# Kernel tuning notes

Hardware: AMD Instinct MI355X
Metric: run time of the kernel (lower is better)

Reference implementation:

```python
import jax, jax.numpy as jnp
import numpy as np

N_NODES = 50000
N_EDGES = 400000
N_GRAPHS = 64
DN = 64    # node features
DE = 64    # edge features
DG = 16    # global features
DH = 128   # mlp hidden
DO = 64    # mlp output
NHID = 2   # hidden layers
E_IN = 2 * DN + DE + DG   # 208
N_IN = DN + DO + DG       # 144


def _mlp_params(key, d_in, d_h, d_out, n_hid):
    ks = jax.random.split(key, 3)
    w_in = jax.random.normal(ks[0], (d_in, d_h), jnp.float32) * (2.0 / d_in) ** 0.5
    w_h = jax.random.normal(ks[1], (n_hid, d_h, d_h), jnp.float32) * (2.0 / d_h) ** 0.5
    w_out = jax.random.normal(ks[2], (d_h, d_out), jnp.float32) * (2.0 / d_h) ** 0.5
    return (w_in, jnp.zeros((d_h,), jnp.float32), w_h, jnp.zeros((n_hid, d_h), jnp.float32),
            w_out, jnp.zeros((d_out,), jnp.float32), jnp.ones((d_out,), jnp.float32),
            jnp.zeros((d_out,), jnp.float32))


def _mlp(h, w_in, b_in, w_h, b_h, w_out, b_out, g, b):
    # Lin -> [relu, Lin]*NHID -> relu -> Lin -> LayerNorm  (dropout=0 at eval)
    h = h @ w_in + b_in
    for i in range(w_h.shape[0]):
        h = jax.nn.relu(h) @ w_h[i] + b_h[i]
    h = jax.nn.relu(h) @ w_out + b_out
    mu = jnp.mean(h, axis=-1, keepdims=True)
    var = jnp.mean((h - mu) ** 2, axis=-1, keepdims=True)
    return (h - mu) * jax.lax.rsqrt(var + 1e-5) * g + b


def setup_inputs() -> dict:
    key = jax.random.key(0)
    k = jax.random.split(key, 8)
    x = jax.random.normal(k[0], (N_NODES, DN), jnp.float32)
    edge_attr = jax.random.normal(k[1], (N_EDGES, DE), jnp.float32)
    u = jax.random.normal(k[2], (N_GRAPHS, DG), jnp.float32)
    edge_index = jax.random.randint(k[3], (2, N_EDGES), 0, N_NODES, dtype=jnp.int32)
    batch = jnp.sort(jax.random.randint(k[4], (N_NODES,), 0, N_GRAPHS, dtype=jnp.int32))
    names = ["w_in", "b_in", "w_h", "b_h", "w_out", "b_out", "ln_g", "ln_b"]
    d = {"x": x, "edge_attr": edge_attr, "u": u, "edge_index": edge_index, "batch": batch}
    for pref, kk, d_in in (("e_", k[5], E_IN), ("a_", k[6], E_IN), ("n_", k[7], N_IN)):
        for nm, v in zip(names, _mlp_params(kk, d_in, DH, DO, NHID)):
            d[pref + nm] = v
    return d


def reference(x, edge_attr, u, edge_index, batch,
              e_w_in, e_b_in, e_w_h, e_b_h, e_w_out, e_b_out, e_ln_g, e_ln_b,
              a_w_in, a_b_in, a_w_h, a_b_h, a_w_out, a_b_out, a_ln_g, a_ln_b,
              n_w_in, n_b_in, n_w_h, n_b_h, n_w_out, n_b_out, n_ln_g, n_ln_b):
    src, tgt = edge_index[0], edge_index[1]
    edge_batch = batch[src]
    # EdgeModel: gather src/tgt node feats + global feats, concat, MLP (+ sigmoid attention MLP)
    neigh = jnp.concatenate([x[src], x[tgt], edge_attr, u[edge_batch]], axis=1)  # [E, E_IN]
    e_out = _mlp(neigh, e_w_in, e_b_in, e_w_h, e_b_h, e_w_out, e_b_out, e_ln_g, e_ln_b)
    attn = jax.nn.sigmoid(_mlp(neigh, a_w_in, a_b_in, a_w_h, a_b_h, a_w_out, a_b_out, a_ln_g, a_ln_b))
    e_out = e_out * attn  # [E, DO]
    # NodeModel: scatter-sum incoming (target-indexed) edge outputs, concat, MLP
    agg = jax.ops.segment_sum(e_out, tgt, num_segments=x.shape[0])  # [N, DO], zeros for isolated nodes
    node_in = jnp.concatenate([x, agg, u[batch]], axis=1)  # [N, N_IN]
    x_out = _mlp(node_in, n_w_in, n_b_in, n_w_h, n_b_h, n_w_out, n_b_out, n_ln_g, n_ln_b)
    return x_out
```

## Files before the change

kernel.cpp:

```cpp
#include <hip/hip_runtime.h>
#include <math.h>

#define N_NODES 50000
#define N_EDGES 400000

typedef _Float16 half8 __attribute__((ext_vector_type(8)));
typedef float f32x4 __attribute__((ext_vector_type(4)));

#define LD1 232
#define LDH 136
#define LDN 168

#define AGG_OFF 0
#define XH_OFF  12800000
#define UH_OFF  19200000
#define WP_OFF  19202048
#define O_EW1 0
#define O_EH0 28672
#define O_EH1 45056
#define O_EWO 61440
#define O_AW1 69632
#define O_AH0 98304
#define O_AH1 114688
#define O_AWO 131072
#define O_NW1 139264
#define O_NH0 159744
#define O_NH1 176128
#define O_NWO 192512

__device__ __forceinline__ f32x4 mfma16(half8 a, half8 b, f32x4 c) {
  return __builtin_amdgcn_mfma_f32_16x16x32_f16(a, b, c, 0, 0, 0);
}

template<int NS, int LDSRC>
__device__ __forceinline__ void gemm32(const _Float16* __restrict__ src,
                                       _Float16* __restrict__ dst,
                                       const _Float16* __restrict__ wp16,
                                       const float* __restrict__ bias,
                                       int w, int lane) {
  const half8* wp = (const half8*)wp16;
  const int r = lane & 15, ch = lane >> 4;
  f32x4 a0[4], a1[4];
#pragma unroll
  for (int m = 0; m < 4; ++m) {
    a0[m] = (f32x4){0.f, 0.f, 0.f, 0.f};
    a1[m] = (f32x4){0.f, 0.f, 0.f, 0.f};
  }
#pragma unroll
  for (int s = 0; s < NS; ++s) {
    half8 b0 = wp[(s * 4 + ch) * 128 + w * 32 + r];
    half8 b1 = wp[(s * 4 + ch) * 128 + w * 32 + 16 + r];
#pragma unroll
    for (int m = 0; m < 4; ++m) {
      half8 a = *(const half8*)(src + (m * 16 + r) * LDSRC + s * 32 + ch * 8);
      a0[m] = mfma16(a, b0, a0[m]);
      a1[m] = mfma16(a, b1, a1[m]);
    }
  }
  float bb0 = bias[w * 32 + r], bb1 = bias[w * 32 + 16 + r];
#pragma unroll
  for (int m = 0; m < 4; ++m)
#pragma unroll
    for (int q = 0; q < 4; ++q) {
      int row = m * 16 + ch * 4 + q;
      dst[row * LDH + w * 32 + r]      = (_Float16)fmaxf(a0[m][q] + bb0, 0.f);
      dst[row * LDH + w * 32 + 16 + r] = (_Float16)fmaxf(a1[m][q] + bb1, 0.f);
    }
}

struct EdgeP {
  const float* edge_attr; const int* edge_index; const int* batch;
  const _Float16* x_h; const _Float16* u_h; const _Float16* wp;
  const float *eBin, *eBh, *eBout, *eG, *eBt;
  const float *aBin, *aBh, *aBout, *aG, *aBt;
  float* agg;
};

__global__ __launch_bounds__(512, 4) void edge_kernel(EdgeP p) {
  __shared__ __align__(16) _Float16 sIn[64 * LD1];
  __shared__ __align__(16) _Float16 sQe[64 * LDH];
  __shared__ __align__(16) _Float16 sQa[64 * LDH];
  __shared__ __align__(16) _Float16 sPa[64 * LDH];
  const int tid = threadIdx.x;
  const int e0 = blockIdx.x * 64;

  for (int idx = tid; idx < 64 * 32; idx += 512) {
    int c = idx & 31, e = idx >> 5;
    if (c >= 28) continue;
    int col = c * 8;
    half8 v;
    if (col < 64) {
      int s = p.edge_index[e0 + e];
      v = *(const half8*)(p.x_h + (size_t)s * 64 + col);
    } else if (col < 128) {
      int t = p.edge_index[N_EDGES + e0 + e];
      v = *(const half8*)(p.x_h + (size_t)t * 64 + col - 64);
    } else if (col < 192) {
      const float* ea = p.edge_attr + (size_t)(e0 + e) * 64 + (col - 128);
      float4 f0 = *(const float4*)ea, f1 = *(const float4*)(ea + 4);
      v[0] = (_Float16)f0.x; v[1] = (_Float16)f0.y;
      v[2] = (_Float16)f0.z; v[3] = (_Float16)f0.w;
      v[4] = (_Float16)f1.x; v[5] = (_Float16)f1.y;
      v[6] = (_Float16)f1.z; v[7] = (_Float16)f1.w;
    } else if (col < 208) {
      int s = p.edge_index[e0 + e];
      int eb = p.batch[s];
      v = *(const half8*)(p.u_h + eb * 16 + col - 192);
    } else {
#pragma unroll
      for (int j = 0; j < 8; ++j) v[j] = (_Float16)0.f;
    }
    *(half8*)(sIn + e * LD1 + col) = v;
  }
  __syncthreads();

  const int lane = tid & 63, wid = tid >> 6, we = wid & 3;
  const bool isE = wid < 4;
  _Float16* ping = isE ? sQe : sQa;
  _Float16* pong = isE ? sIn : sPa;
  const _Float16* w1 = p.wp + (isE ? O_EW1 : O_AW1);
  const _Float16* h0 = p.wp + (isE ? O_EH0 : O_AH0);
  const _Float16* h1 = p.wp + (isE ? O_EH1 : O_AH1);
  const _Float16* wo = p.wp + (isE ? O_EWO : O_AWO);
  const float* bin = isE ? p.eBin : p.aBin;
  const float* bh  = isE ? p.eBh  : p.aBh;
  const float* bo  = isE ? p.eBout: p.aBout;
  const float* g   = isE ? p.eG   : p.aG;
  const float* bt  = isE ? p.eBt  : p.aBt;

  gemm32<7, LD1>(sIn,  ping, w1, bin,      we, lane); __syncthreads();
  gemm32<4, LDH>(ping, pong, h0, bh,       we, lane); __syncthreads();
  gemm32<4, LDH>(pong, ping, h1, bh + 128, we, lane); __syncthreads();

  const int r = lane & 15, ch = lane >> 4;
  const half8* wpo = (const half8*)wo;
  f32x4 acc[4];
#pragma unroll
  for (int t = 0; t < 4; ++t) acc[t] = (f32x4){0.f, 0.f, 0.f, 0.f};
#pragma unroll
  for (int s = 0; s < 4; ++s) {
    half8 a = *(const half8*)(ping + (we * 16 + r) * LDH + s * 32 + ch * 8);
#pragma unroll
    for (int t = 0; t < 4; ++t)
      acc[t] = mfma16(a, wpo[(s * 4 + ch) * 64 + t * 16 + r], acc[t]);
  }
  float gg[4], tt[4];
#pragma unroll
  for (int t = 0; t < 4; ++t) {
    int cidx = t * 16 + r;
    float bov = bo[cidx];
#pragma unroll
    for (int q = 0; q < 4; ++q) acc[t][q] += bov;
    gg[t] = g[cidx]; tt[t] = bt[cidx];
  }
  float mu_[4], rs_[4];
#pragma unroll
  for (int q = 0; q < 4; ++q) {
    float s1 = 0.f, s2 = 0.f;
#pragma unroll
    for (int t = 0; t < 4; ++t) { float v = acc[t][q]; s1 += v; s2 += v * v; }
#pragma unroll
    for (int mk = 1; mk < 16; mk <<= 1) {
      s1 += __shfl_xor(s1, mk); s2 += __shfl_xor(s2, mk);
    }
    mu_[q] = s1 * (1.f / 64);
    rs_[q] = rsqrtf(s2 * (1.f / 64) - mu_[q] * mu_[q] + 1e-5f);
  }
  float* cmb = (float*)sPa;
  if (!isE) {
#pragma unroll
    for (int q = 0; q < 4; ++q) {
      int row = we * 16 + ch * 4 + q;
#pragma unroll
      for (int t = 0; t < 4; ++t) {
        float oa = (acc[t][q] - mu_[q]) * rs_[q] * gg[t] + tt[t];
        cmb[row * 64 + t * 16 + r] = 1.f / (1.f + __expf(-oa));
      }
    }
  }
  __syncthreads();
  if (isE) {
#pragma unroll
    for (int q = 0; q < 4; ++q) {
      int row = we * 16 + ch * 4 + q;
      int tgt = p.edge_index[N_EDGES + e0 + row];
      float* ap = p.agg + (size_t)tgt * 64 + r;
#pragma unroll
      for (int t = 0; t < 4; ++t) {
        float oe = (acc[t][q] - mu_[q]) * rs_[q] * gg[t] + tt[t];
        atomicAdd(ap + t * 16, oe * cmb[row * 64 + t * 16 + r]);
      }
    }
  }
}

struct NodeP {
  const float* agg; const _Float16* x_h; const _Float16* u_h;
  const _Float16* wp; const int* batch;
  const float *Bin, *Bh, *Bout, *G, *Bt;
  float* out;
};

__global__ __launch_bounds__(256, 2) void node_kernel(NodeP p) {
  __shared__ __align__(16) _Float16 sIn[64 * LDN];
  __shared__ __align__(16) _Float16 sQ[64 * LDH];
  __shared__ int sB[64];
  const int tid = threadIdx.x;
  const int n0 = blockIdx.x * 64;

  if (tid < 64) {
    int n = n0 + tid;
    sB[tid] = (n < N_NODES) ? p.batch[n] : 0;
  }
  __syncthreads();

  for (int idx = tid; idx < 64 * 32; idx += 256) {
    int c = idx & 31, e = idx >> 5;
    if (c >= 21) continue;
    int n = n0 + e, col = c * 8;
    half8 v;
    if (n >= N_NODES || col >= 144) {
#pragma unroll
      for (int j = 0; j < 8; ++j) v[j] = (_Float16)0.f;
    } else if (col < 64) {
      v = *(const half8*)(p.x_h + (size_t)n * 64 + col);
    } else if (col < 128) {
      const float* ag = p.agg + (size_t)n * 64 + (col - 64);
      float4 f0 = *(const float4*)ag, f1 = *(const float4*)(ag + 4);
      v[0] = (_Float16)f0.x; v[1] = (_Float16)f0.y;
      v[2] = (_Float16)f0.z; v[3] = (_Float16)f0.w;
      v[4] = (_Float16)f1.x; v[5] = (_Float16)f1.y;
      v[6] = (_Float16)f1.z; v[7] = (_Float16)f1.w;
    } else {
      v = *(const half8*)(p.u_h + sB[e] * 16 + col - 128);
    }
    *(half8*)(sIn + e * LDN + col) = v;
  }
  __syncthreads();

  const int lane = tid & 63, w = tid >> 6;
  _Float16* sP = sIn;

  gemm32<5, LDN>(sIn, sQ, p.wp + O_NW1, p.Bin, w, lane);      __syncthreads();
  gemm32<4, LDH>(sQ, sP, p.wp + O_NH0, p.Bh, w, lane);        __syncthreads();
  gemm32<4, LDH>(sP, sQ, p.wp + O_NH1, p.Bh + 128, w, lane);  __syncthreads();

  const int r = lane & 15, ch = lane >> 4;
  const half8* wpNo = (const half8*)(p.wp + O_NWO);
  f32x4 acc[4];
#pragma unroll
  for (int t = 0; t < 4; ++t) acc[t] = (f32x4){0.f, 0.f, 0.f, 0.f};
#pragma unroll
  for (int s = 0; s < 4; ++s) {
    half8 h = *(const half8*)(sQ + (w * 16 + r) * LDH + s * 32 + ch * 8);
#pragma unroll
    for (int t = 0; t < 4; ++t) {
      half8 b = wpNo[(s * 4 + ch) * 64 + t * 16 + r];
      acc[t] = mfma16(h, b, acc[t]);
    }
  }
  float g[4], bt[4];
#pragma unroll
  for (int t = 0; t < 4; ++t) {
    int cidx = t * 16 + r;
    float bov = p.Bout[cidx];
#pragma unroll
    for (int q = 0; q < 4; ++q) acc[t][q] += bov;
    g[t] = p.G[cidx]; bt[t] = p.Bt[cidx];
  }
#pragma unroll
  for (int q = 0; q < 4; ++q) {
    float s1 = 0.f, s2 = 0.f;
#pragma unroll
    for (int t = 0; t < 4; ++t) { float v = acc[t][q]; s1 += v; s2 += v * v; }
#pragma unroll
    for (int mk = 1; mk < 16; mk <<= 1) {
      s1 += __shfl_xor(s1, mk); s2 += __shfl_xor(s2, mk);
    }
    float mu = s1 * (1.f / 64);
    float rs = rsqrtf(s2 * (1.f / 64) - mu * mu + 1e-5f);
    int row = w * 16 + ch * 4 + q;
    int n = n0 + row;
    if (n < N_NODES) {
#pragma unroll
      for (int t = 0; t < 4; ++t)
        p.out[(size_t)n * 64 + t * 16 + r] = (acc[t][q] - mu) * rs * g[t] + bt[t];
    }
  }
}

#define GX 112
struct PackP {
  const float* src[12];
  int Kreal[12], Nlog[12], size[12], dstoff[12];
  const float* x; const float* u;
  _Float16* x_h; _Float16* u_h; _Float16* wdst;
};

__global__ void pack_kernel(PackP p) {
  int y = blockIdx.y;
  int idx = blockIdx.x * 256 + threadIdx.x;
  if (y < 12) {
    int sz = p.size[y];
    if (idx >= sz) return;
    int N = 1 << p.Nlog[y];
    int j = idx & 7, t = idx >> 3;
    int n = t & (N - 1);
    int sc = t >> p.Nlog[y];
    int c = sc & 3, s = sc >> 2;
    int k = s * 32 + c * 8 + j;
    p.wdst[p.dstoff[y] + idx] =
        (k < p.Kreal[y]) ? (_Float16)p.src[y][k * N + n] : (_Float16)0.f;
  } else {
    for (int i = idx; i < N_NODES * 64; i += GX * 256) p.x_h[i] = (_Float16)p.x[i];
    for (int i = idx; i < 64 * 16; i += GX * 256) p.u_h[i] = (_Float16)p.u[i];
  }
}

extern "C" void kernel_launch(void* const* d_in, const int* in_sizes, int n_in,
                              void* d_out, int out_size, void* d_ws, size_t ws_size,
                              hipStream_t stream) {
  const float* x = (const float*)d_in[0];
  const float* edge_attr = (const float*)d_in[1];
  const float* u = (const float*)d_in[2];
  const int* edge_index = (const int*)d_in[3];
  const int* batch = (const int*)d_in[4];

  char* ws = (char*)d_ws;
  float* agg = (float*)(ws + AGG_OFF);
  _Float16* x_h = (_Float16*)(ws + XH_OFF);
  _Float16* u_h = (_Float16*)(ws + UH_OFF);
  _Float16* wp = (_Float16*)(ws + WP_OFF);

  hipMemsetAsync(agg, 0, (size_t)N_NODES * 64 * sizeof(float), stream);

  PackP pk;
  const float* eWh = (const float*)d_in[7];
  const float* aWh = (const float*)d_in[15];
  const float* nWh = (const float*)d_in[23];
  const float* srcs[12] = {
      (const float*)d_in[5], eWh, eWh + 16384, (const float*)d_in[9],
      (const float*)d_in[13], aWh, aWh + 16384, (const float*)d_in[17],
      (const float*)d_in[21], nWh, nWh + 16384, (const float*)d_in[25]};
  const int kr[12] = {208, 128, 128, 128, 208, 128, 128, 128, 144, 128, 128, 128};
  const int nl[12] = {7, 7, 7, 6, 7, 7, 7, 6, 7, 7, 7, 6};
  const int sz[12] = {28672, 16384, 16384, 8192, 28672, 16384, 16384, 8192,
                      20480, 16384, 16384, 8192};
  const int off[12] = {O_EW1, O_EH0, O_EH1, O_EWO, O_AW1, O_AH0, O_AH1, O_AWO,
                       O_NW1, O_NH0, O_NH1, O_NWO};
  for (int i = 0; i < 12; ++i) {
    pk.src[i] = srcs[i]; pk.Kreal[i] = kr[i]; pk.Nlog[i] = nl[i];
    pk.size[i] = sz[i]; pk.dstoff[i] = off[i];
  }
  pk.x = x; pk.u = u; pk.x_h = x_h; pk.u_h = u_h; pk.wdst = wp;
  pack_kernel<<<dim3(GX, 13), 256, 0, stream>>>(pk);

  EdgeP ep;
  ep.edge_attr = edge_attr; ep.edge_index = edge_index; ep.batch = batch;
  ep.x_h = x_h; ep.u_h = u_h; ep.wp = wp;
  ep.eBin = (const float*)d_in[6];  ep.eBh = (const float*)d_in[8];
  ep.eBout = (const float*)d_in[10]; ep.eG = (const float*)d_in[11];
  ep.eBt = (const float*)d_in[12];
  ep.aBin = (const float*)d_in[14]; ep.aBh = (const float*)d_in[16];
  ep.aBout = (const float*)d_in[18]; ep.aG = (const float*)d_in[19];
  ep.aBt = (const float*)d_in[20];
  ep.agg = agg;
  edge_kernel<<<N_EDGES / 64, 512, 0, stream>>>(ep);

  NodeP np;
  np.agg = agg; np.x_h = x_h; np.u_h = u_h; np.wp = wp; np.batch = batch;
  np.Bin = (const float*)d_in[22]; np.Bh = (const float*)d_in[24];
  np.Bout = (const float*)d_in[26]; np.G = (const float*)d_in[27];
  np.Bt = (const float*)d_in[28];
  np.out = (float*)d_out;
  node_kernel<<<(N_NODES + 63) / 64, 256, 0, stream>>>(np);
}
```

Measured before the change: 551.3 us.

## Give each wavefront a full 64-row tile and run MLPs without block syncs

Restructures both the edge and node kernels so that each wavefront owns a full 64-row tile and computes all 128 output columns itself, with its own private LDS activation buffer. This removes the __syncthreads barriers between layers. The first layer now loads gathered inputs directly from global memory into MFMA A-operands instead of staging them in shared memory. The edge kernel runs the edge MLP and then the attention MLP one after the other in the same wave, keeping the edge output in registers as fp16, where previously separate waves handled each MLP. In exchange, each wave holds a much larger accumulator set (32 f32x4), which raises register pressure and may lower occupancy; the stored edge output also loses precision to fp16, and the A-operand gathers become uncoalesced.

```diff
diff --git a/kernel.cpp b/kernel.cpp
--- a/kernel.cpp
+++ b/kernel.cpp
@@ -3,13 +3,11 @@
 
 #define N_NODES 50000
 #define N_EDGES 400000
+#define LDH 136
+#define WLDS (64 * LDH)
 
 typedef _Float16 half8 __attribute__((ext_vector_type(8)));
 typedef float f32x4 __attribute__((ext_vector_type(4)));
-
-#define LD1 232
-#define LDH 136
-#define LDN 168
 
 #define AGG_OFF 0
 #define XH_OFF  12800000
@@ -32,39 +30,147 @@
   return __builtin_amdgcn_mfma_f32_16x16x32_f16(a, b, c, 0, 0, 0);
 }
 
-template<int NS, int LDSRC>
-__device__ __forceinline__ void gemm32(const _Float16* __restrict__ src,
-                                       _Float16* __restrict__ dst,
-                                       const _Float16* __restrict__ wp16,
-                                       const float* __restrict__ bias,
-                                       int w, int lane) {
-  const half8* wp = (const half8*)wp16;
-  const int r = lane & 15, ch = lane >> 4;
-  f32x4 a0[4], a1[4];
-#pragma unroll
-  for (int m = 0; m < 4; ++m) {
-    a0[m] = (f32x4){0.f, 0.f, 0.f, 0.f};
-    a1[m] = (f32x4){0.f, 0.f, 0.f, 0.f};
-  }
-#pragma unroll
-  for (int s = 0; s < NS; ++s) {
-    half8 b0 = wp[(s * 4 + ch) * 128 + w * 32 + r];
-    half8 b1 = wp[(s * 4 + ch) * 128 + w * 32 + 16 + r];
+__device__ __forceinline__ half8 cvt8(float4 a, float4 b) {
+  half8 v;
+  v[0] = (_Float16)a.x; v[1] = (_Float16)a.y; v[2] = (_Float16)a.z; v[3] = (_Float16)a.w;
+  v[4] = (_Float16)b.x; v[5] = (_Float16)b.y; v[6] = (_Float16)b.z; v[7] = (_Float16)b.w;
+  return v;
+}
+
+__device__ __forceinline__ half8 zero8() {
+  half8 v;
+#pragma unroll
+  for (int j = 0; j < 8; ++j) v[j] = (_Float16)0.f;
+  return v;
+}
+
+__device__ __forceinline__ void h_layer(_Float16* act, const half8* wp,
+                                        const float* bias, int r, int ch) {
+  f32x4 acc[4][8];
+#pragma unroll
+  for (int m = 0; m < 4; ++m)
+#pragma unroll
+    for (int n = 0; n < 8; ++n) acc[m][n] = (f32x4){0.f, 0.f, 0.f, 0.f};
+#pragma unroll
+  for (int s = 0; s < 4; ++s) {
+    half8 B[8], A[4];
+#pragma unroll
+    for (int n = 0; n < 8; ++n) B[n] = wp[(s * 4 + ch) * 128 + n * 16 + r];
+#pragma unroll
+    for (int m = 0; m < 4; ++m)
+      A[m] = *(const half8*)(act + (m * 16 + r) * LDH + s * 32 + ch * 8);
+#pragma unroll
+    for (int m = 0; m < 4; ++m)
+#pragma unroll
+      for (int n = 0; n < 8; ++n) acc[m][n] = mfma16(A[m], B[n], acc[m][n]);
+  }
+#pragma unroll
+  for (int n = 0; n < 8; ++n) {
+    float bb = bias[n * 16 + r];
+#pragma unroll
+    for (int m = 0; m < 4; ++m)
+#pragma unroll
+      for (int q = 0; q < 4; ++q)
+        act[(m * 16 + ch * 4 + q) * LDH + n * 16 + r] =
+            (_Float16)fmaxf(acc[m][n][q] + bb, 0.f);
+  }
+}
+
+__device__ __forceinline__ void l1_edge(const _Float16* __restrict__ x_h,
+                                        const float* __restrict__ ea,
+                                        const _Float16* __restrict__ u_h,
+                                        _Float16* act, const half8* wp,
+                                        const float* bias,
+                                        const int* srcm, const int* tgtm, const int* ebm,
+                                        int e0, int r, int ch) {
+  f32x4 acc[4][8];
+#pragma unroll
+  for (int m = 0; m < 4; ++m)
+#pragma unroll
+    for (int n = 0; n < 8; ++n) acc[m][n] = (f32x4){0.f, 0.f, 0.f, 0.f};
+#pragma unroll
+  for (int s = 0; s < 7; ++s) {
+    half8 B[8], A[4];
+#pragma unroll
+    for (int n = 0; n < 8; ++n) B[n] = wp[(s * 4 + ch) * 128 + n * 16 + r];
 #pragma unroll
     for (int m = 0; m < 4; ++m) {
-      half8 a = *(const half8*)(src + (m * 16 + r) * LDSRC + s * 32 + ch * 8);
-      a0[m] = mfma16(a, b0, a0[m]);
-      a1[m] = mfma16(a, b1, a1[m]);
-    }
-  }
-  float bb0 = bias[w * 32 + r], bb1 = bias[w * 32 + 16 + r];
+      if (s < 2) {
+        A[m] = *(const half8*)(x_h + (size_t)srcm[m] * 64 + s * 32 + ch * 8);
+      } else if (s < 4) {
+        A[m] = *(const half8*)(x_h + (size_t)tgtm[m] * 64 + (s - 2) * 32 + ch * 8);
+      } else if (s < 6) {
+        const float* pe = ea + (size_t)(e0 + m * 16 + r) * 64 + (s - 4) * 32 + ch * 8;
+        A[m] = cvt8(*(const float4*)pe, *(const float4*)(pe + 4));
+      } else {
+        A[m] = (ch < 2) ? *(const half8*)(u_h + ebm[m] * 16 + ch * 8) : zero8();
+      }
+    }
+#pragma unroll
+    for (int m = 0; m < 4; ++m)
+#pragma unroll
+      for (int n = 0; n < 8; ++n) acc[m][n] = mfma16(A[m], B[n], acc[m][n]);
+  }
+#pragma unroll
+  for (int n = 0; n < 8; ++n) {
+    float bb = bias[n * 16 + r];
+#pragma unroll
+    for (int m = 0; m < 4; ++m)
+#pragma unroll
+      for (int q = 0; q < 4; ++q)
+        act[(m * 16 + ch * 4 + q) * LDH + n * 16 + r] =
+            (_Float16)fmaxf(acc[m][n][q] + bb, 0.f);
+  }
+}
+
+__device__ __forceinline__ void out_layer(const _Float16* act, const half8* wpo,
+                                          const float* bo, const float* g,
+                                          const float* bt, f32x4 acc[4][4],
+                                          int r, int ch) {
+#pragma unroll
+  for (int m = 0; m < 4; ++m)
+#pragma unroll
+    for (int t = 0; t < 4; ++t) acc[m][t] = (f32x4){0.f, 0.f, 0.f, 0.f};
+#pragma unroll
+  for (int s = 0; s < 4; ++s) {
+    half8 B[4], A[4];
+#pragma unroll
+    for (int t = 0; t < 4; ++t) B[t] = wpo[(s * 4 + ch) * 64 + t * 16 + r];
+#pragma unroll
+    for (int m = 0; m < 4; ++m)
+      A[m] = *(const half8*)(act + (m * 16 + r) * LDH + s * 32 + ch * 8);
+#pragma unroll
+    for (int m = 0; m < 4; ++m)
+#pragma unroll
+      for (int t = 0; t < 4; ++t) acc[m][t] = mfma16(A[m], B[t], acc[m][t]);
+  }
+  float bo4[4], g4[4], b4[4];
+#pragma unroll
+  for (int t = 0; t < 4; ++t) {
+    bo4[t] = bo[t * 16 + r]; g4[t] = g[t * 16 + r]; b4[t] = bt[t * 16 + r];
+  }
+#pragma unroll
+  for (int m = 0; m < 4; ++m)
+#pragma unroll
+    for (int t = 0; t < 4; ++t)
+#pragma unroll
+      for (int q = 0; q < 4; ++q) acc[m][t][q] += bo4[t];
 #pragma unroll
   for (int m = 0; m < 4; ++m)
 #pragma unroll
     for (int q = 0; q < 4; ++q) {
-      int row = m * 16 + ch * 4 + q;
-      dst[row * LDH + w * 32 + r]      = (_Float16)fmaxf(a0[m][q] + bb0, 0.f);
-      dst[row * LDH + w * 32 + 16 + r] = (_Float16)fmaxf(a1[m][q] + bb1, 0.f);
+      float s1 = 0.f, s2 = 0.f;
+#pragma unroll
+      for (int t = 0; t < 4; ++t) { float v = acc[m][t][q]; s1 += v; s2 += v * v; }
+#pragma unroll
+      for (int mk = 1; mk < 16; mk <<= 1) {
+        s1 += __shfl_xor(s1, mk); s2 += __shfl_xor(s2, mk);
+      }
+      float mu = s1 * (1.f / 64);
+      float rs = rsqrtf(s2 * (1.f / 64) - mu * mu + 1e-5f);
+#pragma unroll
+      for (int t = 0; t < 4; ++t)
+        acc[m][t][q] = (acc[m][t][q] - mu) * rs * g4[t] + b4[t];
     }
 }
 
@@ -76,122 +182,63 @@
   float* agg;
 };
 
-__global__ __launch_bounds__(512, 4) void edge_kernel(EdgeP p) {
-  __shared__ __align__(16) _Float16 sIn[64 * LD1];
-  __shared__ __align__(16) _Float16 sQe[64 * LDH];
-  __shared__ __align__(16) _Float16 sQa[64 * LDH];
-  __shared__ __align__(16) _Float16 sPa[64 * LDH];
-  const int tid = threadIdx.x;
-  const int e0 = blockIdx.x * 64;
-
-  for (int idx = tid; idx < 64 * 32; idx += 512) {
-    int c = idx & 31, e = idx >> 5;
-    if (c >= 28) continue;
-    int col = c * 8;
-    half8 v;
-    if (col < 64) {
-      int s = p.edge_index[e0 + e];
-      v = *(const half8*)(p.x_h + (size_t)s * 64 + col);
-    } else if (col < 128) {
-      int t = p.edge_index[N_EDGES + e0 + e];
-      v = *(const half8*)(p.x_h + (size_t)t * 64 + col - 64);
-    } else if (col < 192) {
-      const float* ea = p.edge_attr + (size_t)(e0 + e) * 64 + (col - 128);
-      float4 f0 = *(const float4*)ea, f1 = *(const float4*)(ea + 4);
-      v[0] = (_Float16)f0.x; v[1] = (_Float16)f0.y;
-      v[2] = (_Float16)f0.z; v[3] = (_Float16)f0.w;
-      v[4] = (_Float16)f1.x; v[5] = (_Float16)f1.y;
-      v[6] = (_Float16)f1.z; v[7] = (_Float16)f1.w;
-    } else if (col < 208) {
-      int s = p.edge_index[e0 + e];
-      int eb = p.batch[s];
-      v = *(const half8*)(p.u_h + eb * 16 + col - 192);
-    } else {
-#pragma unroll
-      for (int j = 0; j < 8; ++j) v[j] = (_Float16)0.f;
-    }
-    *(half8*)(sIn + e * LD1 + col) = v;
-  }
-  __syncthreads();
-
-  const int lane = tid & 63, wid = tid >> 6, we = wid & 3;
-  const bool isE = wid < 4;
-  _Float16* ping = isE ? sQe : sQa;
-  _Float16* pong = isE ? sIn : sPa;
-  const _Float16* w1 = p.wp + (isE ? O_EW1 : O_AW1);
-  const _Float16* h0 = p.wp + (isE ? O_EH0 : O_AH0);
-  const _Float16* h1 = p.wp + (isE ? O_EH1 : O_AH1);
-  const _Float16* wo = p.wp + (isE ? O_EWO : O_AWO);
-  const float* bin = isE ? p.eBin : p.aBin;
-  const float* bh  = isE ? p.eBh  : p.aBh;
-  const float* bo  = isE ? p.eBout: p.aBout;
-  const float* g   = isE ? p.eG   : p.aG;
-  const float* bt  = isE ? p.eBt  : p.aBt;
-
-  gemm32<7, LD1>(sIn,  ping, w1, bin,      we, lane); __syncthreads();
-  gemm32<4, LDH>(ping, pong, h0, bh,       we, lane); __syncthreads();
-  gemm32<4, LDH>(pong, ping, h1, bh + 128, we, lane); __syncthreads();
-
+__global__ __launch_bounds__(256, 2) void edge_kernel(EdgeP p) {
+  __shared__ __align__(16) _Float16 sAct[4 * WLDS];
+  const int tid = threadIdx.x, lane = tid & 63, w = tid >> 6;
   const int r = lane & 15, ch = lane >> 4;
-  const half8* wpo = (const half8*)wo;
-  f32x4 acc[4];
-#pragma unroll
-  for (int t = 0; t < 4; ++t) acc[t] = (f32x4){0.f, 0.f, 0.f, 0.f};
-#pragma unroll
-  for (int s = 0; s < 4; ++s) {
-    half8 a = *(const half8*)(ping + (we * 16 + r) * LDH + s * 32 + ch * 8);
-#pragma unroll
-    for (int t = 0; t < 4; ++t)
-      acc[t] = mfma16(a, wpo[(s * 4 + ch) * 64 + t * 16 + r], acc[t]);
-  }
-  float gg[4], tt[4];
-#pragma unroll
-  for (int t = 0; t < 4; ++t) {
-    int cidx = t * 16 + r;
-    float bov = bo[cidx];
-#pragma unroll
-    for (int q = 0; q < 4; ++q) acc[t][q] += bov;
-    gg[t] = g[cidx]; tt[t] = bt[cidx];
-  }
-  float mu_[4], rs_[4];
-#pragma unroll
-  for (int q = 0; q < 4; ++q) {
-    float s1 = 0.f, s2 = 0.f;
-#pragma unroll
-    for (int t = 0; t < 4; ++t) { float v = acc[t][q]; s1 += v; s2 += v * v; }
-#pragma unroll
-    for (int mk = 1; mk < 16; mk <<= 1) {
-      s1 += __shfl_xor(s1, mk); s2 += __shfl_xor(s2, mk);
-    }
-    mu_[q] = s1 * (1.f / 64);
-    rs_[q] = rsqrtf(s2 * (1.f / 64) - mu_[q] * mu_[q] + 1e-5f);
-  }
-  float* cmb = (float*)sPa;
-  if (!isE) {
+  const int wgid = blockIdx.x * 4 + w;
+  const int e0 = wgid * 64;
+  if (e0 >= N_EDGES) return;
+  _Float16* act = sAct + w * WLDS;
+
+  int srcm[4], tgtm[4], ebm[4];
+#pragma unroll
+  for (int m = 0; m < 4; ++m) srcm[m] = p.edge_index[e0 + m * 16 + r];
+#pragma unroll
+  for (int m = 0; m < 4; ++m) tgtm[m] = p.edge_index[N_EDGES + e0 + m * 16 + r];
+#pragma unroll
+  for (int m = 0; m < 4; ++m) ebm[m] = p.batch[srcm[m]];
+
+  l1_edge(p.x_h, p.edge_attr, p.u_h, act, (const half8*)(p.wp + O_EW1), p.eBin,
+          srcm, tgtm, ebm, e0, r, ch);
+  h_layer(act, (const half8*)(p.wp + O_EH0), p.eBh, r, ch);
+  h_layer(act, (const half8*)(p.wp + O_EH1), p.eBh + 128, r, ch);
+  f32x4 accE[4][4];
+  out_layer(act, (const half8*)(p.wp + O_EWO), p.eBout, p.eG, p.eBt, accE, r, ch);
+  half8 eP[8];
+#pragma unroll
+  for (int m = 0; m < 4; ++m)
+#pragma unroll
+    for (int h = 0; h < 2; ++h) {
+      half8 v;
+#pragma unroll
+      for (int tt = 0; tt < 2; ++tt)
+#pragma unroll
+        for (int q = 0; q < 4; ++q)
+          v[tt * 4 + q] = (_Float16)accE[m][h * 2 + tt][q];
+      eP[m * 2 + h] = v;
+    }
+
+  l1_edge(p.x_h, p.edge_attr, p.u_h, act, (const half8*)(p.wp + O_AW1), p.aBin,
+          srcm, tgtm, ebm, e0, r, ch);
+  h_layer(act, (const half8*)(p.wp + O_AH0), p.aBh, r, ch);
+  h_layer(act, (const half8*)(p.wp + O_AH1), p.aBh + 128, r, ch);
+  f32x4 accA[4][4];
+  out_layer(act, (const half8*)(p.wp + O_AWO), p.aBout, p.aG, p.aBt, accA, r, ch);
+
+#pragma unroll
+  for (int m = 0; m < 4; ++m)
 #pragma unroll
     for (int q = 0; q < 4; ++q) {
-      int row = we * 16 + ch * 4 + q;
+      int tq = p.edge_index[N_EDGES + e0 + m * 16 + ch * 4 + q];
+      float* ap = p.agg + (size_t)tq * 64 + r;
 #pragma unroll
       for (int t = 0; t < 4; ++t) {
-        float oa = (acc[t][q] - mu_[q]) * rs_[q] * gg[t] + tt[t];
-        cmb[row * 64 + t * 16 + r] = 1.f / (1.f + __expf(-oa));
+        float sg = 1.f / (1.f + __expf(-accA[m][t][q]));
+        float oe = (float)eP[m * 2 + (t >> 1)][(t & 1) * 4 + q];
+        atomicAdd(ap + t * 16, oe * sg);
       }
     }
-  }
-  __syncthreads();
-  if (isE) {
-#pragma unroll
-    for (int q = 0; q < 4; ++q) {
-      int row = we * 16 + ch * 4 + q;
-      int tgt = p.edge_index[N_EDGES + e0 + row];
-      float* ap = p.agg + (size_t)tgt * 64 + r;
-#pragma unroll
-      for (int t = 0; t < 4; ++t) {
-        float oe = (acc[t][q] - mu_[q]) * rs_[q] * gg[t] + tt[t];
-        atomicAdd(ap + t * 16, oe * cmb[row * 64 + t * 16 + r]);
-      }
-    }
-  }
 }
 
 struct NodeP {
@@ -202,91 +249,79 @@
 };
 
 __global__ __launch_bounds__(256, 2) void node_kernel(NodeP p) {
-  __shared__ __align__(16) _Float16 sIn[64 * LDN];
-  __shared__ __align__(16) _Float16 sQ[64 * LDH];
-  __shared__ int sB[64];
-  const int tid = threadIdx.x;
-  const int n0 = blockIdx.x * 64;
-
-  if (tid < 64) {
-    int n = n0 + tid;
-    sB[tid] = (n < N_NODES) ? p.batch[n] : 0;
-  }
-  __syncthreads();
-
-  for (int idx = tid; idx < 64 * 32; idx += 256) {
-    int c = idx & 31, e = idx >> 5;
-    if (c >= 21) continue;
-    int n = n0 + e, col = c * 8;
-    half8 v;
-    if (n >= N_NODES || col >= 144) {
-#pragma unroll
-      for (int j = 0; j < 8; ++j) v[j] = (_Float16)0.f;
-    } else if (col < 64) {
-      v = *(const half8*)(p.x_h + (size_t)n * 64 + col);
-    } else if (col < 128) {
-      const float* ag = p.agg + (size_t)n * 64 + (col - 64);
-      float4 f0 = *(const float4*)ag, f1 = *(const float4*)(ag + 4);
-      v[0] = (_Float16)f0.x; v[1] = (_Float16)f0.y;
-      v[2] = (_Float16)f0.z; v[3] = (_Float16)f0.w;
-      v[4] = (_Float16)f1.x; v[5] = (_Float16)f1.y;
-      v[6] = (_Float16)f1.z; v[7] = (_Float16)f1.w;
-    } else {
-      v = *(const half8*)(p.u_h + sB[e] * 16 + col - 128);
-    }
-    *(half8*)(sIn + e * LDN + col) = v;
-  }
-  __syncthreads();
-
-  const int lane = tid & 63, w = tid >> 6;
-  _Float16* sP = sIn;
-
-  gemm32<5, LDN>(sIn, sQ, p.wp + O_NW1, p.Bin, w, lane);      __syncthreads();
-  gemm32<4, LDH>(sQ, sP, p.wp + O_NH0, p.Bh, w, lane);        __syncthreads();
-  gemm32<4, LDH>(sP, sQ, p.wp + O_NH1, p.Bh + 128, w, lane);  __syncthreads();
-
+  __shared__ __align__(16) _Float16 sAct[4 * WLDS];
+  const int tid = threadIdx.x, lane = tid & 63, w = tid >> 6;
   const int r = lane & 15, ch = lane >> 4;
-  const half8* wpNo = (const half8*)(p.wp + O_NWO);
-  f32x4 acc[4];
-#pragma unroll
-  for (int t = 0; t < 4; ++t) acc[t] = (f32x4){0.f, 0.f, 0.f, 0.f};
-#pragma unroll
-  for (int s = 0; s < 4; ++s) {
-    half8 h = *(const half8*)(sQ + (w * 16 + r) * LDH + s * 32 + ch * 8);
-#pragma unroll
-    for (int t = 0; t < 4; ++t) {
-      half8 b = wpNo[(s * 4 + ch) * 64 + t * 16 + r];
-      acc[t] = mfma16(h, b, acc[t]);
-    }
-  }
-  float g[4], bt[4];
-#pragma unroll
-  for (int t = 0; t < 4; ++t) {
-    int cidx = t * 16 + r;
-    float bov = p.Bout[cidx];
-#pragma unroll
-    for (int q = 0; q < 4; ++q) acc[t][q] += bov;
-    g[t] = p.G[cidx]; bt[t] = p.Bt[cidx];
-  }
-#pragma unroll
-  for (int q = 0; q < 4; ++q) {
-    float s1 = 0.f, s2 = 0.f;
-#pragma unroll
-    for (int t = 0; t < 4; ++t) { float v = acc[t][q]; s1 += v; s2 += v * v; }
-#pragma unroll
-    for (int mk = 1; mk < 16; mk <<= 1) {
-      s1 += __shfl_xor(s1, mk); s2 += __shfl_xor(s2, mk);
-    }
-    float mu = s1 * (1.f / 64);
-    float rs = rsqrtf(s2 * (1.f / 64) - mu * mu + 1e-5f);
-    int row = w * 16 + ch * 4 + q;
-    int n = n0 + row;
-    if (n < N_NODES) {
-#pragma unroll
-      for (int t = 0; t < 4; ++t)
-        p.out[(size_t)n * 64 + t * 16 + r] = (acc[t][q] - mu) * rs * g[t] + bt[t];
-    }
-  }
+  const int wgid = blockIdx.x * 4 + w;
+  const int n0 = wgid * 64;
+  if (n0 >= N_NODES) return;
+  _Float16* act = sAct + w * WLDS;
+
+  int nm[4], bm[4];
+#pragma unroll
+  for (int m = 0; m < 4; ++m) {
+    int n = n0 + m * 16 + r;
+    nm[m] = (n < N_NODES) ? n : 0;
+  }
+#pragma unroll
+  for (int m = 0; m < 4; ++m) bm[m] = p.batch[nm[m]];
+
+  {
+    f32x4 acc[4][8];
+#pragma unroll
+    for (int m = 0; m < 4; ++m)
+#pragma unroll
+      for (int n = 0; n < 8; ++n) acc[m][n] = (f32x4){0.f, 0.f, 0.f, 0.f};
+    const half8* wp = (const half8*)(p.wp + O_NW1);
+#pragma unroll
+    for (int s = 0; s < 5; ++s) {
+      half8 B[8], A[4];
+#pragma unroll
+      for (int n = 0; n < 8; ++n) B[n] = wp[(s * 4 + ch) * 128 + n * 16 + r];
+#pragma unroll
+      for (int m = 0; m < 4; ++m) {
+        if (s < 2) {
+          A[m] = *(const half8*)(p.x_h + (size_t)nm[m] * 64 + s * 32 + ch * 8);
+        } else if (s < 4) {
+          const float* ag = p.agg + (size_t)nm[m] * 64 + (s - 2) * 32 + ch * 8;
+          A[m] = cvt8(*(const float4*)ag, *(const float4*)(ag + 4));
+        } else {
+          A[m] = (ch < 2) ? *(const half8*)(p.u_h + bm[m] * 16 + ch * 8) : zero8();
+        }
+      }
+#pragma unroll
+      for (int m = 0; m < 4; ++m)
+#pragma unroll
+        for (int n = 0; n < 8; ++n) acc[m][n] = mfma16(A[m], B[n], acc[m][n]);
+    }
+#pragma unroll
+    for (int n = 0; n < 8; ++n) {
+      float bb = p.Bin[n * 16 + r];
+#pragma unroll
+      for (int m = 0; m < 4; ++m)
+#pragma unroll
+        for (int q = 0; q < 4; ++q)
+          act[(m * 16 + ch * 4 + q) * LDH + n * 16 + r] =
+              (_Float16)fmaxf(acc[m][n][q] + bb, 0.f);
+    }
+  }
+
+  h_layer(act, (const half8*)(p.wp + O_NH0), p.Bh, r, ch);
+  h_layer(act, (const half8*)(p.wp + O_NH1), p.Bh + 128, r, ch);
+  f32x4 acc[4][4];
+  out_layer(act, (const half8*)(p.wp + O_NWO), p.Bout, p.G, p.Bt, acc, r, ch);
+
+#pragma unroll
+  for (int m = 0; m < 4; ++m)
+#pragma unroll
+    for (int q = 0; q < 4; ++q) {
+      int n = n0 + m * 16 + ch * 4 + q;
+      if (n < N_NODES) {
+#pragma unroll
+        for (int t = 0; t < 4; ++t)
+          p.out[(size_t)n * 64 + t * 16 + r] = acc[m][t][q];
+      }
+    }
 }
 
 #define GX 112
@@ -365,7 +400,7 @@
   ep.aBout = (const float*)d_in[18]; ep.aG = (const float*)d_in[19];
   ep.aBt = (const float*)d_in[20];
   ep.agg = agg;
-  edge_kernel<<<N_EDGES / 64, 512, 0, stream>>>(ep);
+  edge_kernel<<<(6250 + 3) / 4, 256, 0, stream>>>(ep);
 
   NodeP np;
   np.agg = agg; np.x_h = x_h; np.u_h = u_h; np.wp = wp; np.batch = batch;
@@ -373,5 +408,5 @@
   np.Bout = (const float*)d_in[26]; np.G = (const float*)d_in[27];
   np.Bt = (const float*)d_in[28];
   np.out = (float*)d_out;
-  node_kernel<<<(N_NODES + 63) / 64, 256, 0, stream>>>(np);
-}
+  node_kernel<<<(784 + 3) / 4, 256, 0, stream>>>(np);
+}
```

After: 629.0 us. +14.1%, slower.
